# Kernel optimization log

Measured on AMD Instinct MI355X. Metric: run time of the kernel, lower is better.

Reference implementation:

```python
import jax, jax.numpy as jnp
import numpy as np

NUM_HEADS = 8
LN_EPS = 1e-5


def _ln(x, g, b):
    mu = x.mean(-1, keepdims=True)
    xc = x - mu
    v = (xc * xc).mean(-1, keepdims=True)
    return xc * jax.lax.rsqrt(v + LN_EPS) * g + b


def setup_inputs() -> dict:
    key = jax.random.key(0)
    B, T, D, NI, NT = 16, 512, 256, 85, 77
    L, FF, TH = 2, 1024, 32
    ks = iter(jax.random.split(key, 40))
    def nrm(shape, std):
        return jax.random.normal(next(ks), shape, jnp.float32) * std
    inp = {
        'img_tokens': nrm((B, NI, D), 1.0),
        'text_tokens': nrm((B, NT, D), 1.0),
        'task_tokens': nrm((T, D), 0.02),
        'type_task': nrm((D,), 0.02),
        'type_img': nrm((D,), 0.02),
        'type_txt': nrm((D,), 0.02),
        'in_ln_g': jnp.ones((D,), jnp.float32), 'in_ln_b': jnp.zeros((D,), jnp.float32),
        'Wqkv': nrm((L, 3 * D, D), 1.0 / np.sqrt(D)), 'bqkv': jnp.zeros((L, 3 * D), jnp.float32),
        'Wo': nrm((L, D, D), 1.0 / np.sqrt(D)), 'bo': jnp.zeros((L, D), jnp.float32),
        'ln1_g': jnp.ones((L, D), jnp.float32), 'ln1_b': jnp.zeros((L, D), jnp.float32),
        'ln2_g': jnp.ones((L, D), jnp.float32), 'ln2_b': jnp.zeros((L, D), jnp.float32),
        'W1': nrm((L, FF, D), 1.0 / np.sqrt(D)), 'b1': jnp.zeros((L, FF), jnp.float32),
        'W2': nrm((L, D, FF), 1.0 / np.sqrt(FF)), 'b2': jnp.zeros((L, D), jnp.float32),
        'out_ln_g': jnp.ones((D,), jnp.float32), 'out_ln_b': jnp.zeros((D,), jnp.float32),
        'tw1': nrm((T, TH, D), 1.0 / np.sqrt(D)), 'tb1': jnp.zeros((T, TH), jnp.float32),
        'tw2': nrm((T, TH), 1.0 / np.sqrt(TH)), 'tb2': jnp.zeros((T,), jnp.float32),
        'text_mask': jnp.arange(NT)[None, :] < jax.random.randint(next(ks), (B, 1), 10, NT + 1),
        'labels': jax.random.randint(next(ks), (B, T), -1, 2),
    }
    return inp


def reference(img_tokens, text_tokens, task_tokens, type_task, type_img, type_txt,
              in_ln_g, in_ln_b, Wqkv, bqkv, Wo, bo, ln1_g, ln1_b, ln2_g, ln2_b,
              W1, b1, W2, b2, out_ln_g, out_ln_b, tw1, tb1, tw2, tb2,
              text_mask, labels):
    B, NI, D = img_tokens.shape
    T = task_tokens.shape[0]
    L = Wqkv.shape[0]
    hd = D // NUM_HEADS
    available = labels != -1                                   # (B, T)
    n_avail = available.sum(axis=1)                            # (B,)
    # Route B: stable-sort available task ids to the front (permutation per row)
    order = jnp.argsort((~available).astype(jnp.int32), axis=1, stable=True)  # (B, T)
    task_toks = task_tokens[order] + type_task                 # (B, T, D)
    seq = jnp.concatenate([task_toks, img_tokens + type_img, text_tokens + type_txt], axis=1)
    seq = _ln(seq, in_ln_g, in_ln_b)
    task_pad = jnp.arange(T)[None, :] >= n_avail[:, None]
    pad = jnp.concatenate([task_pad, jnp.zeros((B, NI), bool), ~text_mask], axis=1)
    bias = jnp.where(pad, -1e9, 0.0).astype(seq.dtype)[:, None, None, :]  # key-padding mask
    scale = 1.0 / np.sqrt(hd)
    S = seq.shape[1]
    for l in range(L):  # pre-LN transformer encoder layers (eval mode)
        h = _ln(seq, ln1_g[l], ln1_b[l])
        qkv = h @ Wqkv[l].T + bqkv[l]
        q, k, v = jnp.split(qkv, 3, axis=-1)
        q = q.reshape(B, S, NUM_HEADS, hd)
        k = k.reshape(B, S, NUM_HEADS, hd)
        v = v.reshape(B, S, NUM_HEADS, hd)
        scores = jnp.einsum('bqhd,bkhd->bhqk', q, k) * scale + bias
        attn = jax.nn.softmax(scores, axis=-1)
        o = jnp.einsum('bhqk,bkhd->bqhd', attn, v).reshape(B, S, D)
        seq = seq + o @ Wo[l].T + bo[l]
        h2 = _ln(seq, ln2_g[l], ln2_b[l])
        seq = seq + jax.nn.gelu(h2 @ W1[l].T + b1[l], approximate=False) @ W2[l].T + b2[l]
    task_out = _ln(seq[:, :T], out_ln_g, out_ln_b)             # (B, T, D)
    # undo the per-row permutation so task t's token sits at column t, then
    # apply all per-task towers as one grouped matmul (MoE dispatch/combine)
    y = jnp.zeros_like(task_out).at[jnp.arange(B)[:, None], order].set(task_out)
    hsz = jax.nn.relu(jnp.einsum('btd,thd->bth', y, tw1) + tb1[None])
    out = jnp.einsum('bth,th->bt', hsz, tw2) + tb2[None]
    return jnp.where(available, out, jnp.zeros((), out.dtype))
```

## Files before the change

kernel.cpp:

```cpp
#include <hip/hip_runtime.h>
#include <hip/hip_bf16.h>
#include <math.h>

constexpr int B_  = 16;
constexpr int T_  = 512;
constexpr int D_  = 256;
constexpr int NI_ = 85;
constexpr int NT_ = 77;
constexpr int S_  = T_ + NI_ + NT_;
constexpr int M_  = B_ * S_;
constexpr int FF_ = 1024;
constexpr int TH_ = 32;
constexpr int NH_ = 8;
constexpr int KT_ = 704;
constexpr int NKT_ = KT_ / 64;

constexpr float MASK_NEG = -30000.0f;

constexpr int N_FT = 26;
constexpr int OFF_[N_FT + 1] = {
    0,
    348160,
    663552,
    794624,
    794880,
    795136,
    795392,
    795648,
    795904,
    1189120,
    1190656,
    1321728,
    1322240,
    1322752,
    1323264,
    1323776,
    1324288,
    1848576,
    1850624,
    2374912,
    2375424,
    2375680,
    2375936,
    6570240,
    6586624,
    6603008,
    6603520
};
constexpr int TOTAL_ELEMS = OFF_[N_FT];
constexpr int CONV_BLOCKS = (TOTAL_ELEMS + 511) / 512;

typedef __attribute__((ext_vector_type(8))) short bfrag;
typedef __attribute__((ext_vector_type(4))) float f32x4;

__device__ inline float bf2f(__hip_bfloat16 x) { return __bfloat162float(x); }
__device__ inline __hip_bfloat16 f2bf(float x) { return __float2bfloat16(x); }
__device__ inline float wsum64(float v) {
    #pragma unroll
    for (int m = 32; m >= 1; m >>= 1) v += __shfl_xor(v, m, 64);
    return v;
}
__device__ inline bool is_f32_mode(const void* ln_g_raw) {
    return (*(const unsigned int*)ln_g_raw) == 0x3F800000u;
}

__device__ inline bool tile_dead(int m0, int m1, const int* __restrict__ n_avail) {
    int b = m0 / S_;
    int base = b * S_;
    return (m0 >= base + n_avail[b]) && (m1 <= base + T_);
}

__device__ inline void gload_lds16(const __hip_bfloat16* g, __hip_bfloat16* l) {
#if defined(__has_builtin) && __has_builtin(__builtin_amdgcn_global_load_lds)
    __builtin_amdgcn_global_load_lds(
        (const __attribute__((address_space(1))) unsigned int*)g,
        (__attribute__((address_space(3))) unsigned int*)l, 16, 0, 0);
#else
    *reinterpret_cast<uint4*>(l) = *reinterpret_cast<const uint4*>(g);
#endif
}

struct Ptrs { const void* p[N_FT]; };

__global__ __launch_bounds__(512) void k_init(Ptrs ptrs, __hip_bfloat16* __restrict__ canon,
                                              const int* __restrict__ labels,
                                              int* __restrict__ inv,
                                              int* __restrict__ n_avail) {
    if (blockIdx.x < CONV_BLOCKS) {
        int idx = blockIdx.x * 512 + threadIdx.x;
        if (idx >= TOTAL_ELEMS) return;
        bool f32 = is_f32_mode(ptrs.p[6]);
        int t = 0;
        #pragma unroll
        for (int i = 1; i < N_FT; i++) if (idx >= OFF_[i]) t = i;
        int local = idx - OFF_[t];
        if (f32) canon[idx] = f2bf(((const float*)ptrs.p[t])[local]);
        else     canon[idx] = ((const __hip_bfloat16*)ptrs.p[t])[local];
    } else {
        __shared__ int sc[T_];
        int b = blockIdx.x - CONV_BLOCKS, t = threadIdx.x;
        int av = (labels[b * T_ + t] != -1) ? 1 : 0;
        sc[t] = av;
        __syncthreads();
        for (int off = 1; off < T_; off <<= 1) {
            int v = sc[t];
            int u = (t >= off) ? sc[t - off] : 0;
            __syncthreads();
            sc[t] = v + u;
            __syncthreads();
        }
        int incl  = sc[t];
        int excl  = incl - av;
        int total = sc[T_ - 1];
        inv[b * T_ + t] = av ? excl : (total + (t - excl));
        if (t == 0) n_avail[b] = total;
    }
}

__global__ void k_build(const __hip_bfloat16* __restrict__ img,
                        const __hip_bfloat16* __restrict__ txt,
                        const __hip_bfloat16* __restrict__ task,
                        const __hip_bfloat16* __restrict__ ty_task,
                        const __hip_bfloat16* __restrict__ ty_img,
                        const __hip_bfloat16* __restrict__ ty_txt,
                        const __hip_bfloat16* __restrict__ g,
                        const __hip_bfloat16* __restrict__ bln,
                        const __hip_bfloat16* __restrict__ g1,
                        const __hip_bfloat16* __restrict__ b1,
                        const void* __restrict__ text_mask,
                        const int* __restrict__ inv,
                        const int* __restrict__ n_avail,
                        float* __restrict__ seq,
                        __hip_bfloat16* __restrict__ h1,
                        float* __restrict__ bias) {
    int blk = blockIdx.x;
    int b = blk / S_, j = blk % S_;
    int lane = threadIdx.x;

    int dest;
    float bias_v;
    const __hip_bfloat16* src;
    const __hip_bfloat16* tvec;
    if (j < T_) {
        dest = inv[b * T_ + j];
        src = task + (size_t)j * D_;
        tvec = ty_task;
        bias_v = (dest >= n_avail[b]) ? MASK_NEG : 0.f;
    } else if (j < T_ + NI_) {
        dest = j;
        src = img + (size_t)(b * NI_ + (j - T_)) * D_;
        tvec = ty_img;
        bias_v = 0.f;
    } else {
        int x2 = j - T_ - NI_;
        dest = j;
        src = txt + (size_t)(b * NT_ + x2) * D_;
        tvec = ty_txt;
        const unsigned char* mb = (const unsigned char*)text_mask;
        bool is_byte = (mb[1] != 0);
        int mv = is_byte ? (int)mb[b * NT_ + x2]
                         : ((const int*)text_mask)[b * NT_ + x2];
        bias_v = mv ? 0.f : MASK_NEG;
    }

    float x[4];
    float s = 0.f, ss = 0.f;
    #pragma unroll
    for (int i = 0; i < 4; i++) {
        int d = lane * 4 + i;
        x[i] = bf2f(src[d]) + bf2f(tvec[d]);
        s += x[i];
        ss += x[i] * x[i];
    }
    s = wsum64(s);
    ss = wsum64(ss);
    float mean = s * (1.f / D_);
    float var  = ss * (1.f / D_) - mean * mean;
    float r    = rsqrtf(fmaxf(var, 0.f) + 1e-5f);

    float y[4];
    float s2 = 0.f, ss2 = 0.f;
    float* orow = seq + ((size_t)b * S_ + dest) * D_;
    #pragma unroll
    for (int i = 0; i < 4; i++) {
        int d = lane * 4 + i;
        y[i] = (x[i] - mean) * r * bf2f(g[d]) + bf2f(bln[d]);
        orow[d] = y[i];
        s2 += y[i];
        ss2 += y[i] * y[i];
    }
    s2 = wsum64(s2);
    ss2 = wsum64(ss2);
    float mean2 = s2 * (1.f / D_);
    float var2  = ss2 * (1.f / D_) - mean2 * mean2;
    float r2    = rsqrtf(fmaxf(var2, 0.f) + 1e-5f);
    __hip_bfloat16 tmp[4];
    #pragma unroll
    for (int i = 0; i < 4; i++) {
        int d = lane * 4 + i;
        tmp[i] = f2bf((y[i] - mean2) * r2 * bf2f(g1[d]) + bf2f(b1[d]));
    }
    *reinterpret_cast<uint2*>(h1 + ((size_t)b * S_ + dest) * D_ + lane * 4) =
        *reinterpret_cast<uint2*>(tmp);
    if (lane == 0) bias[b * S_ + dest] = bias_v;
}

template <int GELU>
__global__ __launch_bounds__(256) void k_gemm(const __hip_bfloat16* __restrict__ A,
                                              const __hip_bfloat16* __restrict__ W,
                                              const __hip_bfloat16* __restrict__ bias,
                                              __hip_bfloat16* __restrict__ Cout,
                                              const int* __restrict__ n_avail,
                                              int Mm, int N, int K) {
    __shared__ __align__(16) unsigned char Sh[24576];
    __hip_bfloat16* As = (__hip_bfloat16*)Sh;
    __hip_bfloat16* Ws = (__hip_bfloat16*)(Sh + 8192);
    __hip_bfloat16* Es = (__hip_bfloat16*)Sh;

    int m0 = blockIdx.x * 64;
    if (tile_dead(m0, m0 + 64, n_avail)) return;
    int n0 = blockIdx.y * 128;
    int tid = threadIdx.x;
    int w = tid >> 6, lane = tid & 63;
    int lrow = lane & 15, quad = lane >> 4;

    f32x4 acc[8] = {};

    int kq = (tid & 7) * 8;
    int arow = tid >> 3;
    const __hip_bfloat16* Ar0 = A + (size_t)min(m0 + arow,      Mm - 1) * K + kq;
    const __hip_bfloat16* Ar1 = A + (size_t)min(m0 + arow + 32, Mm - 1) * K + kq;
    __hip_bfloat16* Al0 = As + tid * 8;
    __hip_bfloat16* Al1 = As + (tid + 256) * 8;
    const __hip_bfloat16* Wr[4];
    __hip_bfloat16* Wl[4];
    #pragma unroll
    for (int i = 0; i < 4; i++) {
        int c = tid + i * 256;
        Wr[i] = W + (size_t)(n0 + (c >> 3)) * K + kq;
        Wl[i] = Ws + c * 8;
    }

    for (int k0 = 0; k0 < K; k0 += 64) {
        __syncthreads();
        gload_lds16(Ar0 + k0, Al0);
        gload_lds16(Ar1 + k0, Al1);
        #pragma unroll
        for (int i = 0; i < 4; i++) gload_lds16(Wr[i] + k0, Wl[i]);
        __syncthreads();

        #pragma unroll
        for (int ko = 0; ko < 2; ko++) {
            bfrag af = *reinterpret_cast<const bfrag*>(&As[(w * 16 + lrow) * 64 + ko * 32 + quad * 8]);
            #pragma unroll
            for (int nt = 0; nt < 8; nt++) {
                bfrag bf = *reinterpret_cast<const bfrag*>(&Ws[(nt * 16 + lrow) * 64 + ko * 32 + quad * 8]);
                acc[nt] = __builtin_amdgcn_mfma_f32_16x16x32_bf16(af, bf, acc[nt], 0, 0, 0);
            }
        }
    }
    __syncthreads();

    #pragma unroll
    for (int nt = 0; nt < 8; nt++) {
        int col = nt * 16 + lrow;
        float bv = bf2f(bias[n0 + col]);
        #pragma unroll
        for (int rg = 0; rg < 4; rg++) {
            int row = w * 16 + quad * 4 + rg;
            float v = acc[nt][rg] + bv;
            if (GELU) v = 0.5f * v * (1.f + erff(v * 0.70710678118654752f));
            Es[row * 136 + col] = f2bf(v);
        }
    }
    __syncthreads();

    #pragma unroll
    for (int i = 0; i < 4; i++) {
        int c = tid + i * 256;
        int row = c >> 4, off = (c & 15) * 8;
        int gm = m0 + row;
        if (gm < Mm) {
            uint4 v4 = *reinterpret_cast<const uint4*>(&Es[row * 136 + off]);
            *reinterpret_cast<uint4*>(&Cout[(size_t)gm * N + n0 + off]) = v4;
        }
    }
}

template <int LNOUT>
__global__ __launch_bounds__(256) void k_gemm_lnres(const __hip_bfloat16* __restrict__ A,
                                                    const __hip_bfloat16* __restrict__ W,
                                                    const __hip_bfloat16* __restrict__ bias,
                                                    float* __restrict__ seq,
                                                    const __hip_bfloat16* __restrict__ lng,
                                                    const __hip_bfloat16* __restrict__ lnb,
                                                    __hip_bfloat16* __restrict__ lnout,
                                                    const int* __restrict__ n_avail,
                                                    int K) {
    constexpr int N = 256;
    constexpr int ESTRIDE = 260;
    __shared__ __align__(16) unsigned char Sh[36864];
    __hip_bfloat16* As = (__hip_bfloat16*)Sh;
    __hip_bfloat16* Ws = (__hip_bfloat16*)(Sh + 4096);
    float*          Es = (float*)Sh;

    int m0 = blockIdx.x * 32;
    if (tile_dead(m0, m0 + 32, n_avail)) return;
    int tid = threadIdx.x;
    int w = tid >> 6, lane = tid & 63;
    int lrow = lane & 15, quad = lane >> 4;

    f32x4 acc[2][4] = {};

    int kq = (tid & 7) * 8;
    const __hip_bfloat16* Ar = A + (size_t)(m0 + (tid >> 3)) * K + kq;
    __hip_bfloat16* Al = As + tid * 8;
    const __hip_bfloat16* Wr[8];
    __hip_bfloat16* Wl[8];
    #pragma unroll
    for (int i = 0; i < 8; i++) {
        int c = tid + i * 256;
        Wr[i] = W + (size_t)(c >> 3) * K + kq;
        Wl[i] = Ws + c * 8;
    }

    for (int k0 = 0; k0 < K; k0 += 64) {
        __syncthreads();
        gload_lds16(Ar + k0, Al);
        #pragma unroll
        for (int i = 0; i < 8; i++) gload_lds16(Wr[i] + k0, Wl[i]);
        __syncthreads();

        #pragma unroll
        for (int ko = 0; ko < 2; ko++) {
            bfrag af[2], bf[4];
            #pragma unroll
            for (int mt = 0; mt < 2; mt++)
                af[mt] = *reinterpret_cast<const bfrag*>(&As[(mt * 16 + lrow) * 64 + ko * 32 + quad * 8]);
            #pragma unroll
            for (int nt = 0; nt < 4; nt++)
                bf[nt] = *reinterpret_cast<const bfrag*>(&Ws[(w * 64 + nt * 16 + lrow) * 64 + ko * 32 + quad * 8]);
            #pragma unroll
            for (int mt = 0; mt < 2; mt++)
                #pragma unroll
                for (int nt = 0; nt < 4; nt++)
                    acc[mt][nt] = __builtin_amdgcn_mfma_f32_16x16x32_bf16(af[mt], bf[nt], acc[mt][nt], 0, 0, 0);
        }
    }
    __syncthreads();

    #pragma unroll
    for (int nt = 0; nt < 4; nt++) {
        int col = w * 64 + nt * 16 + lrow;
        float bv = bf2f(bias[col]);
        #pragma unroll
        for (int mt = 0; mt < 2; mt++)
            #pragma unroll
            for (int rg = 0; rg < 4; rg++)
                Es[(mt * 16 + quad * 4 + rg) * ESTRIDE + col] = acc[mt][nt][rg] + bv;
    }
    __syncthreads();

    int row = tid >> 3, part = tid & 7;
    size_t gm = (size_t)(m0 + row);
    float* seqrow = seq + gm * N + part * 32;
    float t[32];
    float s = 0.f, ss = 0.f;
    #pragma unroll
    for (int j = 0; j < 8; j++) {
        float4 e = *reinterpret_cast<const float4*>(&Es[row * ESTRIDE + part * 32 + j * 4]);
        float4 r4 = *reinterpret_cast<const float4*>(&seqrow[j * 4]);
        float v0 = e.x + r4.x, v1 = e.y + r4.y, v2 = e.z + r4.z, v3 = e.w + r4.w;
        t[j * 4 + 0] = v0; t[j * 4 + 1] = v1; t[j * 4 + 2] = v2; t[j * 4 + 3] = v3;
        s += v0 + v1 + v2 + v3;
        ss += v0 * v0 + v1 * v1 + v2 * v2 + v3 * v3;
    }
    #pragma unroll
    for (int j = 0; j < 8; j++) {
        float4 o = make_float4(t[j * 4 + 0], t[j * 4 + 1], t[j * 4 + 2], t[j * 4 + 3]);
        *reinterpret_cast<float4*>(&seqrow[j * 4]) = o;
    }
    if (LNOUT) {
        #pragma unroll
        for (int mm = 4; mm >= 1; mm >>= 1) {
            s  += __shfl_xor(s,  mm, 8);
            ss += __shfl_xor(ss, mm, 8);
        }
        float mean = s * (1.f / N);
        float var  = ss * (1.f / N) - mean * mean;
        float r    = rsqrtf(fmaxf(var, 0.f) + 1e-5f);
        __hip_bfloat16 ob[32];
        #pragma unroll
        for (int j = 0; j < 32; j++) {
            int col = part * 32 + j;
            ob[j] = f2bf((t[j] - mean) * r * bf2f(lng[col]) + bf2f(lnb[col]));
        }
        #pragma unroll
        for (int j = 0; j < 4; j++)
            *reinterpret_cast<uint4*>(&lnout[gm * N + part * 32 + j * 8]) =
                *reinterpret_cast<const uint4*>(&ob[j * 8]);
    }
}

__global__ __launch_bounds__(256) void k_fattn(const __hip_bfloat16* __restrict__ qkv,
                                               const float* __restrict__ bias,
                                               const int* __restrict__ n_avail,
                                               __hip_bfloat16* __restrict__ out) {
    __shared__ __align__(16) __hip_bfloat16 Vt[2][32 * 72];
    __shared__ __align__(16) __hip_bfloat16 Ps[4][32 * 72];
    __shared__ float Bs[KT_];
    __shared__ int alive[NKT_];
    __shared__ int tlist[NKT_ + 1];
    __shared__ int nact_s;
    int b = blockIdx.z, h = blockIdx.y;
    int q0b = blockIdx.x * 128;
    if (q0b >= n_avail[b] && q0b + 128 <= T_) return;
    int tid = threadIdx.x;
    int wave = tid >> 6, lane = tid & 63;
    int lrow = lane & 15, quad = lane >> 4;
    int q0 = q0b + wave * 32;

    const float scale = 0.17677669529663687f;
    const __hip_bfloat16* base = qkv + (size_t)b * S_ * 768;
    const float* brow = bias + b * S_;

    if (tid < NKT_) alive[tid] = 0;
    __syncthreads();
    for (int i = tid; i < KT_; i += 256) {
        float v = (i < S_) ? brow[i] : MASK_NEG;
        Bs[i] = v;
        if (v != MASK_NEG) alive[i >> 6] = 1;
    }
    __syncthreads();
    if (tid == 0) {
        int n = 0;
        for (int t = 0; t < NKT_; t++) if (alive[t]) tlist[n++] = t;
        if (n == 0) { tlist[0] = 0; n = 1; }
        tlist[n] = tlist[n - 1];
        nact_s = n;
    }
    __syncthreads();
    int nact = nact_s;

    bfrag qf[2];
    {
        int qr0 = min(q0 + lrow, S_ - 1);
        int qr1 = min(q0 + 16 + lrow, S_ - 1);
        qf[0] = *reinterpret_cast<const bfrag*>(base + (size_t)qr0 * 768 + h * 32 + quad * 8);
        qf[1] = *reinterpret_cast<const bfrag*>(base + (size_t)qr1 * 768 + h * 32 + quad * 8);
    }

    bfrag ones_f;
    #pragma unroll
    for (int i = 0; i < 8; i++) ((short*)&ones_f)[i] = (short)0x3F80;

    float m[2][4];
    #pragma unroll
    for (int qh = 0; qh < 2; qh++)
        #pragma unroll
        for (int rg = 0; rg < 4; rg++) m[qh][rg] = -3e38f;
    f32x4 Lacc[2] = {};
    f32x4 O[2][2] = {};

    int skey = lane;
    int sd   = wave * 8;

    bfrag kf_cur[4], vv_cur;
    {
        int k0 = tlist[0] * 64;
        #pragma unroll
        for (int nt = 0; nt < 4; nt++) {
            int kr = min(k0 + nt * 16 + lrow, S_ - 1);
            kf_cur[nt] = *reinterpret_cast<const bfrag*>(base + (size_t)kr * 768 + 256 + h * 32 + quad * 8);
        }
        int kr = min(k0 + skey, S_ - 1);
        vv_cur = *reinterpret_cast<const bfrag*>(base + (size_t)kr * 768 + 512 + h * 32 + sd);
    }

    for (int i = 0; i < nact; i++) {
        int k0 = tlist[i] * 64;
        __hip_bfloat16* vb = Vt[i & 1];

        #pragma unroll
        for (int j = 0; j < 8; j++) vb[(sd + j) * 72 + skey] = ((const __hip_bfloat16*)&vv_cur)[j];
        __syncthreads();

        bfrag kf_nxt[4], vv_nxt;
        {
            int kb = tlist[i + 1] * 64;
            #pragma unroll
            for (int nt = 0; nt < 4; nt++) {
                int kr = min(kb + nt * 16 + lrow, S_ - 1);
                kf_nxt[nt] = *reinterpret_cast<const bfrag*>(base + (size_t)kr * 768 + 256 + h * 32 + quad * 8);
            }
            int kr = min(kb + skey, S_ - 1);
            vv_nxt = *reinterpret_cast<const bfrag*>(base + (size_t)kr * 768 + 512 + h * 32 + sd);
        }

        f32x4 sc[2][4];
        #pragma unroll
        for (int nt = 0; nt < 4; nt++) {
            float bv = Bs[k0 + nt * 16 + lrow];
            #pragma unroll
            for (int qh = 0; qh < 2; qh++) {
                f32x4 z = {};
                sc[qh][nt] = __builtin_amdgcn_mfma_f32_16x16x32_bf16(qf[qh], kf_cur[nt], z, 0, 0, 0);
                #pragma unroll
                for (int rg = 0; rg < 4; rg++) sc[qh][nt][rg] = sc[qh][nt][rg] * scale + bv;
            }
        }

        #pragma unroll
        for (int qh = 0; qh < 2; qh++) {
            float alpha[4];
            #pragma unroll
            for (int rg = 0; rg < 4; rg++) {
                float rm = fmaxf(fmaxf(sc[qh][0][rg], sc[qh][1][rg]), fmaxf(sc[qh][2][rg], sc[qh][3][rg]));
                #pragma unroll
                for (int mm2 = 1; mm2 <= 8; mm2 <<= 1) rm = fmaxf(rm, __shfl_xor(rm, mm2, 64));
                float mn = fmaxf(m[qh][rg], rm);
                alpha[rg] = __expf(m[qh][rg] - mn);
                m[qh][rg] = mn;
                #pragma unroll
                for (int nt = 0; nt < 4; nt++) sc[qh][nt][rg] = __expf(sc[qh][nt][rg] - mn);
            }
            #pragma unroll
            for (int rg = 0; rg < 4; rg++) {
                O[qh][0][rg] *= alpha[rg];
                O[qh][1][rg] *= alpha[rg];
                Lacc[qh][rg] *= alpha[rg];
            }
            #pragma unroll
            for (int nt = 0; nt < 4; nt++)
                #pragma unroll
                for (int rg = 0; rg < 4; rg++)
                    Ps[wave][(qh * 16 + quad * 4 + rg) * 72 + nt * 16 + lrow] = f2bf(sc[qh][nt][rg]);
        }

        #pragma unroll
        for (int qh = 0; qh < 2; qh++) {
            bfrag ap0 = *reinterpret_cast<const bfrag*>(&Ps[wave][(qh * 16 + lrow) * 72 + quad * 8]);
            bfrag ap1 = *reinterpret_cast<const bfrag*>(&Ps[wave][(qh * 16 + lrow) * 72 + 32 + quad * 8]);
            #pragma unroll
            for (int dt = 0; dt < 2; dt++) {
                bfrag bv0 = *reinterpret_cast<const bfrag*>(&vb[(dt * 16 + lrow) * 72 + quad * 8]);
                bfrag bv1 = *reinterpret_cast<const bfrag*>(&vb[(dt * 16 + lrow) * 72 + 32 + quad * 8]);
                O[qh][dt] = __builtin_amdgcn_mfma_f32_16x16x32_bf16(ap0, bv0, O[qh][dt], 0, 0, 0);
                O[qh][dt] = __builtin_amdgcn_mfma_f32_16x16x32_bf16(ap1, bv1, O[qh][dt], 0, 0, 0);
            }
            Lacc[qh] = __builtin_amdgcn_mfma_f32_16x16x32_bf16(ap0, ones_f, Lacc[qh], 0, 0, 0);
            Lacc[qh] = __builtin_amdgcn_mfma_f32_16x16x32_bf16(ap1, ones_f, Lacc[qh], 0, 0, 0);
        }

        #pragma unroll
        for (int nt = 0; nt < 4; nt++) kf_cur[nt] = kf_nxt[nt];
        vv_cur = vv_nxt;
    }

    #pragma unroll
    for (int qh = 0; qh < 2; qh++)
        #pragma unroll
        for (int rg = 0; rg < 4; rg++) {
            int qrow = q0 + qh * 16 + quad * 4 + rg;
            if (qrow < S_) {
                float invl = 1.f / Lacc[qh][rg];
                #pragma unroll
                for (int dt = 0; dt < 2; dt++)
                    out[((size_t)b * S_ + qrow) * D_ + h * 32 + dt * 16 + lrow] = f2bf(O[qh][dt][rg] * invl);
            }
        }
}

__global__ __launch_bounds__(256) void k_final(const float* __restrict__ seq,
                                               const int* __restrict__ inv,
                                               const int* __restrict__ labels,
                                               const __hip_bfloat16* __restrict__ g,
                                               const __hip_bfloat16* __restrict__ bb,
                                               const __hip_bfloat16* __restrict__ tw1,
                                               const __hip_bfloat16* __restrict__ tb1,
                                               const __hip_bfloat16* __restrict__ tw2,
                                               const __hip_bfloat16* __restrict__ tb2,
                                               const void* __restrict__ ln_g_raw,
                                               void* __restrict__ out) {
    int idx = blockIdx.x;
    int t = idx >> 4, b = idx & 15;
    int tid = threadIdx.x;
    bool f32o = is_f32_mode(ln_g_raw);

    int lab = labels[b * T_ + t];
    if (lab == -1) {
        if (tid == 0) {
            if (f32o) ((float*)out)[b * T_ + t] = 0.f;
            else      ((__hip_bfloat16*)out)[b * T_ + t] = f2bf(0.f);
        }
        return;
    }

    __shared__ float y[D_];
    __shared__ float hb[TH_];
    __shared__ float rs[4], rq[4];

    int row = inv[b * T_ + t];
    float x = seq[((size_t)b * S_ + row) * D_ + tid];
    float s1 = wsum64(x);
    float s2 = wsum64(x * x);
    int w = tid >> 6, lane = tid & 63;
    if (lane == 0) { rs[w] = s1; rq[w] = s2; }
    __syncthreads();
    float fs = rs[0] + rs[1] + rs[2] + rs[3];
    float fq = rq[0] + rq[1] + rq[2] + rq[3];
    float mean = fs * (1.f / D_);
    float var  = fq * (1.f / D_) - mean * mean;
    float r    = rsqrtf(fmaxf(var, 0.f) + 1e-5f);
    y[tid] = (x - mean) * r * bf2f(g[tid]) + bf2f(bb[tid]);
    __syncthreads();

    int hh = tid >> 3, part = tid & 7;
    const uint4* w4 = reinterpret_cast<const uint4*>(tw1 + ((size_t)t * TH_ + hh) * D_ + part * 32);
    float acc = 0.f;
    #pragma unroll
    for (int i = 0; i < 4; i++) {
        uint4 kv = w4[i];
        unsigned int wd[4] = {kv.x, kv.y, kv.z, kv.w};
        #pragma unroll
        for (int j2 = 0; j2 < 4; j2++) {
            unsigned int lo = wd[j2] << 16, hi = wd[j2] & 0xffff0000u;
            float flo, fhi;
            __builtin_memcpy(&flo, &lo, 4);
            __builtin_memcpy(&fhi, &hi, 4);
            acc += y[part * 32 + i * 8 + j2 * 2] * flo;
            acc += y[part * 32 + i * 8 + j2 * 2 + 1] * fhi;
        }
    }
    #pragma unroll
    for (int mm = 4; mm >= 1; mm >>= 1) acc += __shfl_down(acc, mm, 8);
    if (part == 0) {
        float hz = acc + bf2f(tb1[t * TH_ + hh]);
        hz = fmaxf(hz, 0.f);
        hb[hh] = hz * bf2f(tw2[t * TH_ + hh]);
    }
    __syncthreads();
    if (tid == 0) {
        float o = bf2f(tb2[t]);
        #pragma unroll
        for (int i = 0; i < TH_; i++) o += hb[i];
        if (f32o) ((float*)out)[b * T_ + t] = o;
        else      ((__hip_bfloat16*)out)[b * T_ + t] = f2bf(o);
    }
}

extern "C" void kernel_launch(void* const* d_in, const int* in_sizes, int n_in,
                              void* d_out, int out_size, void* d_ws, size_t ws_size,
                              hipStream_t stream) {
    const void* tmask  = d_in[26];
    const int*  labels = (const int*)d_in[27];

    char* p = (char*)d_ws;
    auto alloc = [&](size_t bytes) {
        char* r = p;
        p += (bytes + 255) & ~size_t(255);
        return r;
    };
    __hip_bfloat16* canon  = (__hip_bfloat16*)alloc(sizeof(__hip_bfloat16) * (size_t)TOTAL_ELEMS);
    int*            inv     = (int*)alloc(sizeof(int) * B_ * T_);
    int*            n_avail = (int*)alloc(sizeof(int) * B_);
    float*          bias    = (float*)alloc(sizeof(float) * M_);
    float*          seqF    = (float*)alloc(sizeof(float) * (size_t)M_ * D_);
    __hip_bfloat16* bufA    = (__hip_bfloat16*)alloc(sizeof(__hip_bfloat16) * (size_t)M_ * D_);
    __hip_bfloat16* bufBig  = (__hip_bfloat16*)alloc(sizeof(__hip_bfloat16) * (size_t)M_ * FF_);

    Ptrs ptrs;
    for (int i = 0; i < N_FT; i++) ptrs.p[i] = d_in[i];
    hipLaunchKernelGGL(k_init, dim3(CONV_BLOCKS + B_), dim3(512), 0, stream,
                       ptrs, canon, labels, inv, n_avail);

    const __hip_bfloat16* img      = canon + OFF_[0];
    const __hip_bfloat16* txt      = canon + OFF_[1];
    const __hip_bfloat16* task     = canon + OFF_[2];
    const __hip_bfloat16* ty_task  = canon + OFF_[3];
    const __hip_bfloat16* ty_img   = canon + OFF_[4];
    const __hip_bfloat16* ty_txt   = canon + OFF_[5];
    const __hip_bfloat16* in_ln_g  = canon + OFF_[6];
    const __hip_bfloat16* in_ln_b  = canon + OFF_[7];
    const __hip_bfloat16* Wqkv     = canon + OFF_[8];
    const __hip_bfloat16* bqkv     = canon + OFF_[9];
    const __hip_bfloat16* Wo       = canon + OFF_[10];
    const __hip_bfloat16* bo       = canon + OFF_[11];
    const __hip_bfloat16* ln1_g    = canon + OFF_[12];
    const __hip_bfloat16* ln1_b    = canon + OFF_[13];
    const __hip_bfloat16* ln2_g    = canon + OFF_[14];
    const __hip_bfloat16* ln2_b    = canon + OFF_[15];
    const __hip_bfloat16* W1       = canon + OFF_[16];
    const __hip_bfloat16* b1       = canon + OFF_[17];
    const __hip_bfloat16* W2       = canon + OFF_[18];
    const __hip_bfloat16* b2       = canon + OFF_[19];
    const __hip_bfloat16* out_ln_g = canon + OFF_[20];
    const __hip_bfloat16* out_ln_b = canon + OFF_[21];
    const __hip_bfloat16* tw1      = canon + OFF_[22];
    const __hip_bfloat16* tb1      = canon + OFF_[23];
    const __hip_bfloat16* tw2      = canon + OFF_[24];
    const __hip_bfloat16* tb2      = canon + OFF_[25];

    hipLaunchKernelGGL(k_build, dim3(B_ * S_), dim3(64), 0, stream,
                       img, txt, task, ty_task, ty_img, ty_txt, in_ln_g, in_ln_b,
                       ln1_g, ln1_b, tmask, inv, n_avail, seqF, bufA, bias);

    const int mtiles = (M_ + 63) / 64;
    const int rtiles = M_ / 32;
    const int qtiles = (S_ + 127) / 128;

    for (int l = 0; l < 2; l++) {
        hipLaunchKernelGGL((k_gemm<0>), dim3(mtiles, 6), dim3(256), 0, stream,
                           bufA, Wqkv + (size_t)l * 3 * D_ * D_, bqkv + l * 3 * D_,
                           bufBig, n_avail, M_, 3 * D_, D_);
        hipLaunchKernelGGL(k_fattn, dim3(qtiles, NH_, B_), dim3(256), 0, stream,
                           bufBig, bias, n_avail, bufA);
        hipLaunchKernelGGL((k_gemm_lnres<1>), dim3(rtiles), dim3(256), 0, stream,
                           bufA, Wo + (size_t)l * D_ * D_, bo + l * D_, seqF,
                           ln2_g + l * D_, ln2_b + l * D_, bufA, n_avail, D_);
        hipLaunchKernelGGL((k_gemm<1>), dim3(mtiles, 8), dim3(256), 0, stream,
                           bufA, W1 + (size_t)l * FF_ * D_, b1 + l * FF_,
                           bufBig, n_avail, M_, FF_, D_);
        if (l == 0) {
            hipLaunchKernelGGL((k_gemm_lnres<1>), dim3(rtiles), dim3(256), 0, stream,
                               bufBig, W2 + (size_t)l * D_ * FF_, b2 + l * D_, seqF,
                               ln1_g + 1 * D_, ln1_b + 1 * D_, bufA, n_avail, FF_);
        } else {
            hipLaunchKernelGGL((k_gemm_lnres<0>), dim3(rtiles), dim3(256), 0, stream,
                               bufBig, W2 + (size_t)l * D_ * FF_, b2 + l * D_, seqF,
                               (const __hip_bfloat16*)nullptr, (const __hip_bfloat16*)nullptr,
                               (__hip_bfloat16*)nullptr, n_avail, FF_);
        }
    }

    hipLaunchKernelGGL(k_final, dim3(T_ * B_), dim3(256), 0, stream,
                       seqF, inv, labels, out_ln_g, out_ln_b,
                       tw1, tb1, tw2, tb2, d_in[6], d_out);
}
```

Baseline: 391.6 us.

## Double-buffer LDS tiles in both GEMM kernels to overlap loads with MFMA

Measured after the change: 388.2 us. No clear change (-0.9%).

```diff
diff --git a/kernel.cpp b/kernel.cpp
--- a/kernel.cpp
+++ b/kernel.cpp
@@ -212,10 +212,9 @@
                                               __hip_bfloat16* __restrict__ Cout,
                                               const int* __restrict__ n_avail,
                                               int Mm, int N, int K) {
-    __shared__ __align__(16) unsigned char Sh[24576];
-    __hip_bfloat16* As = (__hip_bfloat16*)Sh;
-    __hip_bfloat16* Ws = (__hip_bfloat16*)(Sh + 8192);
-    __hip_bfloat16* Es = (__hip_bfloat16*)Sh;
+    constexpr int HALF = 12288;
+    __shared__ __align__(16) __hip_bfloat16 Sh[2 * HALF];
+    __hip_bfloat16* Es = Sh;
 
     int m0 = blockIdx.x * 64;
     if (tile_dead(m0, m0 + 64, n_avail)) return;
@@ -230,36 +229,47 @@
     int arow = tid >> 3;
     const __hip_bfloat16* Ar0 = A + (size_t)min(m0 + arow,      Mm - 1) * K + kq;
     const __hip_bfloat16* Ar1 = A + (size_t)min(m0 + arow + 32, Mm - 1) * K + kq;
-    __hip_bfloat16* Al0 = As + tid * 8;
-    __hip_bfloat16* Al1 = As + (tid + 256) * 8;
     const __hip_bfloat16* Wr[4];
-    __hip_bfloat16* Wl[4];
-    #pragma unroll
-    for (int i = 0; i < 4; i++) {
-        int c = tid + i * 256;
-        Wr[i] = W + (size_t)(n0 + (c >> 3)) * K + kq;
-        Wl[i] = Ws + c * 8;
-    }
-
-    for (int k0 = 0; k0 < K; k0 += 64) {
-        __syncthreads();
-        gload_lds16(Ar0 + k0, Al0);
-        gload_lds16(Ar1 + k0, Al1);
-        #pragma unroll
-        for (int i = 0; i < 4; i++) gload_lds16(Wr[i] + k0, Wl[i]);
-        __syncthreads();
-
+    #pragma unroll
+    for (int i = 0; i < 4; i++)
+        Wr[i] = W + (size_t)(n0 + ((tid + i * 256) >> 3)) * K + kq;
+
+    const int nsteps = K >> 6;
+
+    {
+        __hip_bfloat16* As0 = Sh;
+        __hip_bfloat16* Ws0 = Sh + 4096;
+        gload_lds16(Ar0, As0 + tid * 8);
+        gload_lds16(Ar1, As0 + (tid + 256) * 8);
+        #pragma unroll
+        for (int i = 0; i < 4; i++) gload_lds16(Wr[i], Ws0 + (tid + i * 256) * 8);
+    }
+    __syncthreads();
+
+    for (int ks = 0; ks < nsteps; ks++) {
+        int curo = (ks & 1) * HALF;
+        if (ks + 1 < nsteps) {
+            int k1 = (ks + 1) << 6;
+            __hip_bfloat16* Asn = Sh + (HALF - curo);
+            __hip_bfloat16* Wsn = Asn + 4096;
+            gload_lds16(Ar0 + k1, Asn + tid * 8);
+            gload_lds16(Ar1 + k1, Asn + (tid + 256) * 8);
+            #pragma unroll
+            for (int i = 0; i < 4; i++) gload_lds16(Wr[i] + k1, Wsn + (tid + i * 256) * 8);
+        }
+        __hip_bfloat16* Asc = Sh + curo;
+        __hip_bfloat16* Wsc = Asc + 4096;
         #pragma unroll
         for (int ko = 0; ko < 2; ko++) {
-            bfrag af = *reinterpret_cast<const bfrag*>(&As[(w * 16 + lrow) * 64 + ko * 32 + quad * 8]);
+            bfrag af = *reinterpret_cast<const bfrag*>(&Asc[(w * 16 + lrow) * 64 + ko * 32 + quad * 8]);
             #pragma unroll
             for (int nt = 0; nt < 8; nt++) {
-                bfrag bf = *reinterpret_cast<const bfrag*>(&Ws[(nt * 16 + lrow) * 64 + ko * 32 + quad * 8]);
+                bfrag bf = *reinterpret_cast<const bfrag*>(&Wsc[(nt * 16 + lrow) * 64 + ko * 32 + quad * 8]);
                 acc[nt] = __builtin_amdgcn_mfma_f32_16x16x32_bf16(af, bf, acc[nt], 0, 0, 0);
             }
         }
-    }
-    __syncthreads();
+        __syncthreads();
+    }
 
     #pragma unroll
     for (int nt = 0; nt < 8; nt++) {
@@ -299,10 +309,9 @@
                                                     int K) {
     constexpr int N = 256;
     constexpr int ESTRIDE = 260;
-    __shared__ __align__(16) unsigned char Sh[36864];
-    __hip_bfloat16* As = (__hip_bfloat16*)Sh;
-    __hip_bfloat16* Ws = (__hip_bfloat16*)(Sh + 4096);
-    float*          Es = (float*)Sh;
+    constexpr int HALF = 18432;
+    __shared__ __align__(16) __hip_bfloat16 Sh[2 * HALF];
+    float* Es = (float*)Sh;
 
     int m0 = blockIdx.x * 32;
     if (tile_dead(m0, m0 + 32, n_avail)) return;
@@ -314,40 +323,51 @@
 
     int kq = (tid & 7) * 8;
     const __hip_bfloat16* Ar = A + (size_t)(m0 + (tid >> 3)) * K + kq;
-    __hip_bfloat16* Al = As + tid * 8;
     const __hip_bfloat16* Wr[8];
-    __hip_bfloat16* Wl[8];
-    #pragma unroll
-    for (int i = 0; i < 8; i++) {
-        int c = tid + i * 256;
-        Wr[i] = W + (size_t)(c >> 3) * K + kq;
-        Wl[i] = Ws + c * 8;
-    }
-
-    for (int k0 = 0; k0 < K; k0 += 64) {
-        __syncthreads();
-        gload_lds16(Ar + k0, Al);
-        #pragma unroll
-        for (int i = 0; i < 8; i++) gload_lds16(Wr[i] + k0, Wl[i]);
-        __syncthreads();
-
+    #pragma unroll
+    for (int i = 0; i < 8; i++)
+        Wr[i] = W + (size_t)((tid + i * 256) >> 3) * K + kq;
+
+    const int nsteps = K >> 6;
+
+    {
+        __hip_bfloat16* As0 = Sh;
+        __hip_bfloat16* Ws0 = Sh + 2048;
+        gload_lds16(Ar, As0 + tid * 8);
+        #pragma unroll
+        for (int i = 0; i < 8; i++) gload_lds16(Wr[i], Ws0 + (tid + i * 256) * 8);
+    }
+    __syncthreads();
+
+    for (int ks = 0; ks < nsteps; ks++) {
+        int curo = (ks & 1) * HALF;
+        if (ks + 1 < nsteps) {
+            int k1 = (ks + 1) << 6;
+            __hip_bfloat16* Asn = Sh + (HALF - curo);
+            __hip_bfloat16* Wsn = Asn + 2048;
+            gload_lds16(Ar + k1, Asn + tid * 8);
+            #pragma unroll
+            for (int i = 0; i < 8; i++) gload_lds16(Wr[i] + k1, Wsn + (tid + i * 256) * 8);
+        }
+        __hip_bfloat16* Asc = Sh + curo;
+        __hip_bfloat16* Wsc = Asc + 2048;
         #pragma unroll
         for (int ko = 0; ko < 2; ko++) {
             bfrag af[2], bf[4];
             #pragma unroll
             for (int mt = 0; mt < 2; mt++)
-                af[mt] = *reinterpret_cast<const bfrag*>(&As[(mt * 16 + lrow) * 64 + ko * 32 + quad * 8]);
+                af[mt] = *reinterpret_cast<const bfrag*>(&Asc[(mt * 16 + lrow) * 64 + ko * 32 + quad * 8]);
             #pragma unroll
             for (int nt = 0; nt < 4; nt++)
-                bf[nt] = *reinterpret_cast<const bfrag*>(&Ws[(w * 64 + nt * 16 + lrow) * 64 + ko * 32 + quad * 8]);
+                bf[nt] = *reinterpret_cast<const bfrag*>(&Wsc[(w * 64 + nt * 16 + lrow) * 64 + ko * 32 + quad * 8]);
             #pragma unroll
             for (int mt = 0; mt < 2; mt++)
                 #pragma unroll
                 for (int nt = 0; nt < 4; nt++)
                     acc[mt][nt] = __builtin_amdgcn_mfma_f32_16x16x32_bf16(af[mt], bf[nt], acc[mt][nt], 0, 0, 0);
         }
-    }
-    __syncthreads();
+        __syncthreads();
+    }
 
     #pragma unroll
     for (int nt = 0; nt < 4; nt++) {
```
